# Optimization experiments

Hardware: AMD Instinct MI355X
Metric: run time of the kernel (lower is better)

The kernel has to match this reference:

```python
import jax, jax.numpy as jnp
import numpy as np

B, N, T, NL, DIM, H, HD = 4, 2048, 8, 64, 1024, 16, 64


def setup_inputs() -> dict:
    key = jax.random.key(0)
    ks = jax.random.split(key, 8)
    text = jax.random.normal(ks[0], (B, N, DIM), dtype=jnp.float32)
    media = jax.random.normal(ks[1], (B, T, NL, DIM), dtype=jnp.float32)
    # place exactly T media tokens per row, evenly spaced, so cumsum times are in [1, T]
    loc = np.zeros((B, N), dtype=bool)
    step = N // T
    loc[:, np.arange(T) * step] = True
    media_locations = jnp.asarray(loc)
    s = 1.0 / np.sqrt(DIM)
    wq = jax.random.normal(ks[2], (DIM, DIM), dtype=jnp.float32) * s
    wkv = jax.random.normal(ks[3], (DIM, 2 * DIM), dtype=jnp.float32) * s
    wo = jax.random.normal(ks[4], (DIM, DIM), dtype=jnp.float32) * s
    bo = jnp.zeros((DIM,), dtype=jnp.float32)
    ln_g = jnp.ones((DIM,), dtype=jnp.float32)
    ln_b = jnp.zeros((DIM,), dtype=jnp.float32)
    return {"text": text, "media": media, "media_locations": media_locations,
            "wq": wq, "wkv": wkv, "wo": wo, "bo": bo, "ln_g": ln_g, "ln_b": ln_b}


def _layernorm(x, g, b, eps=1e-5):
    mu = jnp.mean(x, axis=-1, keepdims=True)
    var = jnp.var(x, axis=-1, keepdims=True)
    return (x - mu) * jax.lax.rsqrt(var + eps) * g + b


def reference(text, media, media_locations, wq, wkv, wo, bo, ln_g, ln_b):
    b, t, nl, d = media.shape
    tn = _layernorm(text, ln_g, ln_b)                 # [b, n, d]
    q = tn @ wq                                        # [b, n, d]
    m = media.reshape(b, t * nl, d)                    # [b, tn, d]
    kv = m @ wkv                                       # [b, tn, 2d]
    k, v = jnp.split(kv, 2, axis=-1)
    q = q.reshape(b, -1, H, HD).transpose(0, 2, 1, 3)  # [b, h, n, hd]
    k = k.reshape(b, -1, H, HD).transpose(0, 2, 1, 3)  # [b, h, tn, hd]
    v = v.reshape(b, -1, H, HD).transpose(0, 2, 1, 3)
    scores = jnp.einsum('bhid,bhjd->bhij', q, k)       # [b, h, n, tn]
    text_times = jnp.cumsum(media_locations.astype(jnp.int32), axis=-1)  # [b, n]
    media_times = jnp.repeat(jnp.arange(1, t + 1, dtype=jnp.int32), nl)  # [tn]
    mask = text_times[:, None, :, None] == media_times[None, None, None, :]
    neg = jnp.finfo(scores.dtype).min
    scores = jnp.where(mask, scores, neg)
    attn = jax.nn.softmax(scores, axis=-1)
    no_media = (text_times == 0)[:, None, :, None]     # [b, 1, n, 1]
    attn = jnp.where(no_media, 0.0, attn)
    out = jnp.einsum('bhij,bhjd->bhid', attn, v)       # [b, h, n, hd]
    out = out.transpose(0, 2, 1, 3).reshape(b, -1, H * HD)
    return out @ wo + bo
```

## Files before the change

### kernel.cpp

```cpp
#include <hip/hip_runtime.h>
#include <stdint.h>

#define B_ 4
#define N_ 2048
#define T_ 8
#define NL_ 64
#define DIM_ 1024
#define H_ 16
#define HD_ 64
#define TN_ (T_*NL_)

typedef __bf16 bf16x8 __attribute__((ext_vector_type(8)));
typedef float f32x4 __attribute__((ext_vector_type(4)));

__device__ __forceinline__ float b2f(unsigned short x) {
  union { uint32_t u; float f; } v; v.u = ((uint32_t)x) << 16; return v.f;
}
__device__ __forceinline__ unsigned short f2b(float f) {
  union { float f; uint32_t u; } v; v.f = f;
  uint32_t r = v.u + 0x7FFFu + ((v.u >> 16) & 1u);
  return (unsigned short)(r >> 16);
}

__device__ __forceinline__ void gload_lds16(const unsigned short* g, unsigned short* l) {
  __builtin_amdgcn_global_load_lds(
      (const __attribute__((address_space(1))) uint32_t*)g,
      (__attribute__((address_space(3))) uint32_t*)l, 16, 0, 0);
}

__global__ void detect_kernel(const unsigned short* __restrict__ text, int* __restrict__ flag) {
  int t = threadIdx.x;
  int bad = 0;
  #pragma unroll
  for (int i = 0; i < 16; i++) {
    unsigned short w = text[t * 16 + i];
    int e = (w >> 7) & 0xFF;
    if (e != 0 && (e < 90 || e > 150)) bad++;
  }
  __shared__ int red[256];
  red[t] = bad;
  __syncthreads();
  for (int o = 128; o > 0; o >>= 1) { if (t < o) red[t] += red[t + o]; __syncthreads(); }
  if (t == 0) flag[0] = (red[0] > 256) ? 1 : 0;
}

#define PREP_TIMES 4
#define PREP_LN    (B_*N_)
#define PREP_CAST  2049
#define PREP_TR    4096

__global__ __launch_bounds__(256) void prep_kernel(
    const void* __restrict__ locs, int* __restrict__ tt,
    const void* __restrict__ text, const void* __restrict__ lng,
    const void* __restrict__ lnb, unsigned short* __restrict__ tn,
    const void* __restrict__ media, unsigned short* __restrict__ mb,
    const void* __restrict__ bo, unsigned short* __restrict__ bob,
    const void* __restrict__ wq, unsigned short* __restrict__ wqt,
    const void* __restrict__ wkv, unsigned short* __restrict__ wkvt,
    const void* __restrict__ wo, unsigned short* __restrict__ wot,
    const int* __restrict__ flag) {
  __shared__ __align__(16) unsigned char shraw[32 * 33 * 2];
  int gb = blockIdx.x;
  int t = threadIdx.x;

  if (gb < PREP_TIMES) {
    int* red = (int*)shraw;
    int b = gb;
    const unsigned char* p8 = (const unsigned char*)locs;
    const int* p32 = (const int*)locs;
    int cnt = 0;
    for (int i = t; i < B_*N_; i += 256) cnt += (p8[i] != 0) ? 1 : 0;
    red[t] = cnt;
    __syncthreads();
    for (int off = 128; off > 0; off >>= 1) {
      if (t < off) red[t] += red[t + off];
      __syncthreads();
    }
    int total = red[0];
    __syncthreads();
    bool isb = (total >= 2 * T_);
    int x[8];
    int base = b * N_ + t * 8;
    if (isb) {
      #pragma unroll
      for (int i = 0; i < 8; i++) x[i] = (int)(p8[base + i] != 0);
    } else {
      #pragma unroll
      for (int i = 0; i < 8; i++) x[i] = (int)(p32[base + i] != 0);
    }
    #pragma unroll
    for (int i = 1; i < 8; i++) x[i] += x[i-1];
    int tot = x[7];
    red[t] = tot;
    __syncthreads();
    for (int off = 1; off < 256; off <<= 1) {
      int v = (t >= off) ? red[t - off] : 0;
      __syncthreads();
      red[t] += v;
      __syncthreads();
    }
    int excl = red[t] - tot;
    #pragma unroll
    for (int i = 0; i < 8; i++) tt[base + i] = excl + x[i];
    return;
  }
  gb -= PREP_TIMES;

  if (gb < PREP_LN) {
    float* sm = (float*)shraw;
    int row = gb;
    bool isf = (*flag != 0);
    float f0, f1, f2, f3, g0, g1, g2, g3, c0, c1, c2, c3;
    if (isf) {
      float4 xv = ((const float4*)text)[(size_t)row * (DIM_/4) + t];
      f0 = xv.x; f1 = xv.y; f2 = xv.z; f3 = xv.w;
      float4 gv = ((const float4*)lng)[t];
      g0 = gv.x; g1 = gv.y; g2 = gv.z; g3 = gv.w;
      float4 bv = ((const float4*)lnb)[t];
      c0 = bv.x; c1 = bv.y; c2 = bv.z; c3 = bv.w;
    } else {
      ushort4 xv = ((const ushort4*)text)[(size_t)row * (DIM_/4) + t];
      f0 = b2f(xv.x); f1 = b2f(xv.y); f2 = b2f(xv.z); f3 = b2f(xv.w);
      ushort4 gv = ((const ushort4*)lng)[t];
      g0 = b2f(gv.x); g1 = b2f(gv.y); g2 = b2f(gv.z); g3 = b2f(gv.w);
      ushort4 bv = ((const ushort4*)lnb)[t];
      c0 = b2f(bv.x); c1 = b2f(bv.y); c2 = b2f(bv.z); c3 = b2f(bv.w);
    }
    float s  = f0 + f1 + f2 + f3;
    float s2 = f0*f0 + f1*f1 + f2*f2 + f3*f3;
    for (int off = 32; off > 0; off >>= 1) { s += __shfl_xor(s, off); s2 += __shfl_xor(s2, off); }
    int wave = t >> 6, lane = t & 63;
    if (lane == 0) { sm[wave] = s; sm[wave + 4] = s2; }
    __syncthreads();
    float ts  = sm[0] + sm[1] + sm[2] + sm[3];
    float ts2 = sm[4] + sm[5] + sm[6] + sm[7];
    float mean = ts * (1.0f / DIM_);
    float var  = ts2 * (1.0f / DIM_) - mean * mean;
    float rs = rsqrtf(var + 1e-5f);
    ushort4 o;
    o.x = f2b((f0 - mean) * rs * g0 + c0);
    o.y = f2b((f1 - mean) * rs * g1 + c1);
    o.z = f2b((f2 - mean) * rs * g2 + c2);
    o.w = f2b((f3 - mean) * rs * g3 + c3);
    ((ushort4*)(tn + (size_t)row * DIM_))[t] = o;
    return;
  }
  gb -= PREP_LN;

  if (gb < PREP_CAST) {
    const int N4M = (B_*T_*NL_*DIM_) / 4;
    int i = gb * 256 + t;
    bool isf = (*flag != 0);
    if (i < N4M) {
      ushort4 o;
      if (isf) {
        float4 v = ((const float4*)media)[i];
        o.x = f2b(v.x); o.y = f2b(v.y); o.z = f2b(v.z); o.w = f2b(v.w);
      } else {
        o = ((const ushort4*)media)[i];
      }
      ((ushort4*)mb)[i] = o;
    } else {
      int j = i - N4M;
      if (j < DIM_/4) {
        ushort4 o;
        if (isf) {
          float4 v = ((const float4*)bo)[j];
          o.x = f2b(v.x); o.y = f2b(v.y); o.z = f2b(v.z); o.w = f2b(v.w);
        } else {
          o = ((const ushort4*)bo)[j];
        }
        ((ushort4*)bob)[j] = o;
      }
    }
    return;
  }
  gb -= PREP_CAST;

  {
    unsigned short (*tile)[33] = (unsigned short (*)[33])shraw;
    const void* src; unsigned short* dst; int C, zz, nx;
    if (gb < 1024)      { src = wq;  dst = wqt;  C = 1024; zz = gb;        nx = 32; }
    else if (gb < 3072) { src = wkv; dst = wkvt; C = 2048; zz = gb - 1024; nx = 64; }
    else                { src = wo;  dst = wot;  C = 1024; zz = gb - 3072; nx = 32; }
    const int R = 1024;
    int xi = zz % nx, yi = zz / nx;
    int bx = xi * 32, by = yi * 32;
    int x = t & 31, y = t >> 5;
    if (*flag) {
      const float* s = (const float*)src;
      for (int i = y; i < 32; i += 8) tile[i][x] = f2b(s[(size_t)(by + i) * C + bx + x]);
    } else {
      const unsigned short* s = (const unsigned short*)src;
      for (int i = y; i < 32; i += 8) tile[i][x] = s[(size_t)(by + i) * C + bx + x];
    }
    __syncthreads();
    for (int i = y; i < 32; i += 8) dst[(size_t)(bx + i) * R + by + x] = tile[x][i];
  }
}

__device__ __forceinline__ void gemm128_core(const unsigned short* __restrict__ A,
                                             const unsigned short* __restrict__ Bt,
                                             unsigned short* __restrict__ C,
                                             float* __restrict__ Cf,
                                             const unsigned short* __restrict__ bias,
                                             int bid, int mtiles, int M, int N, int K,
                                             bool f32o, int t) {
  __shared__ unsigned short As[3][128][32];
  __shared__ unsigned short Bs[3][128][32];
  int m0 = (bid % mtiles) * 128, n0 = (bid / mtiles) * 128;
  int wave = t >> 6, lane = t & 63;
  int wr = wave >> 1, wc = wave & 1;
  f32x4 acc[4][4];
  #pragma unroll
  for (int i = 0; i < 4; i++)
    #pragma unroll
    for (int j = 0; j < 4; j++)
      #pragma unroll
      for (int r = 0; r < 4; r++) acc[i][j][r] = 0.f;
  int lr = lane & 15;
  int lk = (((lane >> 4) ^ ((lr >> 2) & 3)) & 3) * 8;
  int row0 = t >> 2,         kcp0 = (t & 3) * 8;
  int row1 = (t + 256) >> 2, kcp1 = ((t + 256) & 3) * 8;
  int kg0 = (((t & 3) ^ ((row0 >> 2) & 3)) & 3) * 8;
  int kg1 = ((((t + 256) & 3) ^ ((row1 >> 2) & 3)) & 3) * 8;
  const unsigned short* a0 = A  + (size_t)(m0 + row0) * K + kg0;
  const unsigned short* a1 = A  + (size_t)(m0 + row1) * K + kg1;
  const unsigned short* b0 = Bt + (size_t)(n0 + row0) * K + kg0;
  const unsigned short* b1 = Bt + (size_t)(n0 + row1) * K + kg1;
#define STAGE_(buf, koff) do { \
    gload_lds16(a0 + (koff), &As[buf][row0][kcp0]); \
    gload_lds16(a1 + (koff), &As[buf][row1][kcp1]); \
    gload_lds16(b0 + (koff), &Bs[buf][row0][kcp0]); \
    gload_lds16(b1 + (koff), &Bs[buf][row1][kcp1]); \
  } while (0)
  STAGE_(0, 0);
  STAGE_(1, 32);
  STAGE_(2, 64);
  asm volatile("s_waitcnt vmcnt(8)" ::: "memory");
  __builtin_amdgcn_s_barrier();
  int cur = 0;
  for (int k0 = 0; k0 < K; k0 += 32) {
    bf16x8 af[4], bfr[4];
    #pragma unroll
    for (int i = 0; i < 4; i++) af[i]  = *(const bf16x8*)(&As[cur][wr * 64 + i * 16 + lr][lk]);
    #pragma unroll
    for (int j = 0; j < 4; j++) bfr[j] = *(const bf16x8*)(&Bs[cur][wc * 64 + j * 16 + lr][lk]);
    asm volatile("s_waitcnt lgkmcnt(0)" ::: "memory");
    __builtin_amdgcn_sched_barrier(0);
    __builtin_amdgcn_s_barrier();
    if (k0 + 96 < K) {
      STAGE_(cur, k0 + 96);
      __builtin_amdgcn_sched_barrier(0);
    }
    #pragma unroll
    for (int i = 0; i < 4; i++)
      #pragma unroll
      for (int j = 0; j < 4; j++)
        acc[i][j] = __builtin_amdgcn_mfma_f32_16x16x32_bf16(af[i], bfr[j], acc[i][j], 0, 0, 0);
    if (k0 + 96 < K) {
      asm volatile("s_waitcnt vmcnt(8)" ::: "memory");
      __builtin_amdgcn_s_barrier();
    } else if (k0 + 64 < K) {
      asm volatile("s_waitcnt vmcnt(4)" ::: "memory");
      __builtin_amdgcn_s_barrier();
    } else if (k0 + 32 < K) {
      asm volatile("s_waitcnt vmcnt(0)" ::: "memory");
      __builtin_amdgcn_s_barrier();
    }
    cur = (cur == 2) ? 0 : cur + 1;
  }
#undef STAGE_
  int rbase = (lane >> 4) * 4;
  int cbase = lane & 15;
  #pragma unroll
  for (int i = 0; i < 4; i++) {
    #pragma unroll
    for (int j = 0; j < 4; j++) {
      int row = m0 + wr * 64 + i * 16 + rbase;
      int col = n0 + wc * 64 + j * 16 + cbase;
      float bv = bias ? b2f(bias[col]) : 0.f;
      if (f32o) {
        #pragma unroll
        for (int r = 0; r < 4; r++)
          Cf[(size_t)(row + r) * N + col] = acc[i][j][r] + bv;
      } else {
        #pragma unroll
        for (int r = 0; r < 4; r++)
          C[(size_t)(row + r) * N + col] = f2b(acc[i][j][r] + bv);
      }
    }
  }
}

__global__ __launch_bounds__(256) void gemm_qkv(const unsigned short* __restrict__ tn,
                                                const unsigned short* __restrict__ wqt,
                                                unsigned short* __restrict__ qb,
                                                const unsigned short* __restrict__ mb,
                                                const unsigned short* __restrict__ wkvt,
                                                unsigned short* __restrict__ kvb) {
  int bid = blockIdx.x;
  if (bid < 512)
    gemm128_core(tn, wqt, qb, nullptr, nullptr, bid, 64, B_ * N_, DIM_, DIM_, false, threadIdx.x);
  else
    gemm128_core(mb, wkvt, kvb, nullptr, nullptr, bid - 512, 16, B_ * TN_, 2 * DIM_, DIM_, false, threadIdx.x);
}

__global__ __launch_bounds__(256) void gemm_out(const unsigned short* __restrict__ ao,
                                                const unsigned short* __restrict__ wot,
                                                unsigned short* __restrict__ C,
                                                float* __restrict__ Cf,
                                                const unsigned short* __restrict__ bias,
                                                const int* __restrict__ flag) {
  bool f32o = (*flag != 0);
  gemm128_core(ao, wot, C, Cf, bias, blockIdx.x, 64, B_ * N_, DIM_, DIM_, f32o, threadIdx.x);
}

__global__ __launch_bounds__(64) void attn_mfma(const unsigned short* __restrict__ q,
                                                const unsigned short* __restrict__ kv,
                                                const int* __restrict__ tt,
                                                unsigned short* __restrict__ ao) {
  __shared__ unsigned short Vt[64][72];
  __shared__ unsigned short Ps[64][72];
  int bid = blockIdx.x;
  int h  = bid & 15;
  int nt = (bid >> 4) & 31;
  int b  = bid >> 9;
  int bn0 = b * N_ + nt * 64;
  int lane = threadIdx.x & 63;
  int lr = lane & 15;
  int g  = lane >> 4;
  int g8 = g * 8;

  int tv = tt[bn0];
  float vmul = (tv >= 1 && tv <= T_) ? 1.f : 0.f;
  int tvc = tv < 1 ? 1 : (tv > T_ ? T_ : tv);
  int kvrow0 = b * TN_ + (tvc - 1) * NL_;

  const unsigned short* vbase = kv + (size_t)kvrow0 * (2 * DIM_) + DIM_ + h * HD_;
  #pragma unroll
  for (int d0 = 0; d0 < 64; d0 += 8) {
    uint4 v = *(const uint4*)(vbase + (size_t)lane * (2 * DIM_) + d0);
    Vt[d0 + 0][lane] = (unsigned short)(v.x & 0xffff);
    Vt[d0 + 1][lane] = (unsigned short)(v.x >> 16);
    Vt[d0 + 2][lane] = (unsigned short)(v.y & 0xffff);
    Vt[d0 + 3][lane] = (unsigned short)(v.y >> 16);
    Vt[d0 + 4][lane] = (unsigned short)(v.z & 0xffff);
    Vt[d0 + 5][lane] = (unsigned short)(v.z >> 16);
    Vt[d0 + 6][lane] = (unsigned short)(v.w & 0xffff);
    Vt[d0 + 7][lane] = (unsigned short)(v.w >> 16);
  }

  f32x4 S[4][4];
  #pragma unroll
  for (int i = 0; i < 4; i++)
    #pragma unroll
    for (int j = 0; j < 4; j++)
      #pragma unroll
      for (int r = 0; r < 4; r++) S[i][j][r] = 0.f;
  #pragma unroll
  for (int ks = 0; ks < 2; ks++) {
    bf16x8 aQ[4], bK[4];
    #pragma unroll
    for (int mi = 0; mi < 4; mi++)
      aQ[mi] = *(const bf16x8*)(q + (size_t)(bn0 + mi * 16 + lr) * DIM_ + h * HD_ + ks * 32 + g8);
    #pragma unroll
    for (int ni = 0; ni < 4; ni++)
      bK[ni] = *(const bf16x8*)(kv + (size_t)(kvrow0 + ni * 16 + lr) * (2 * DIM_) + h * HD_ + ks * 32 + g8);
    #pragma unroll
    for (int mi = 0; mi < 4; mi++)
      #pragma unroll
      for (int ni = 0; ni < 4; ni++)
        S[mi][ni] = __builtin_amdgcn_mfma_f32_16x16x32_bf16(aQ[mi], bK[ni], S[mi][ni], 0, 0, 0);
  }

  #pragma unroll
  for (int mi = 0; mi < 4; mi++) {
    #pragma unroll
    for (int r = 0; r < 4; r++) {
      float mx = fmaxf(fmaxf(S[mi][0][r], S[mi][1][r]), fmaxf(S[mi][2][r], S[mi][3][r]));
      mx = fmaxf(mx, __shfl_xor(mx, 1));
      mx = fmaxf(mx, __shfl_xor(mx, 2));
      mx = fmaxf(mx, __shfl_xor(mx, 4));
      mx = fmaxf(mx, __shfl_xor(mx, 8));
      float e0 = __expf(S[mi][0][r] - mx);
      float e1 = __expf(S[mi][1][r] - mx);
      float e2 = __expf(S[mi][2][r] - mx);
      float e3 = __expf(S[mi][3][r] - mx);
      float sum = e0 + e1 + e2 + e3;
      sum += __shfl_xor(sum, 1);
      sum += __shfl_xor(sum, 2);
      sum += __shfl_xor(sum, 4);
      sum += __shfl_xor(sum, 8);
      float inv = 1.f / sum;
      int qrow = mi * 16 + g * 4 + r;
      Ps[qrow][ 0 + lr] = f2b(e0 * inv);
      Ps[qrow][16 + lr] = f2b(e1 * inv);
      Ps[qrow][32 + lr] = f2b(e2 * inv);
      Ps[qrow][48 + lr] = f2b(e3 * inv);
    }
  }
  __syncthreads();

  f32x4 O[4][4];
  #pragma unroll
  for (int i = 0; i < 4; i++)
    #pragma unroll
    for (int j = 0; j < 4; j++)
      #pragma unroll
      for (int r = 0; r < 4; r++) O[i][j][r] = 0.f;
  #pragma unroll
  for (int ks = 0; ks < 2; ks++) {
    bf16x8 aP[4], bV[4];
    #pragma unroll
    for (int mi = 0; mi < 4; mi++)
      aP[mi] = *(const bf16x8*)(&Ps[mi * 16 + lr][ks * 32 + g8]);
    #pragma unroll
    for (int ni = 0; ni < 4; ni++)
      bV[ni] = *(const bf16x8*)(&Vt[ni * 16 + lr][ks * 32 + g8]);
    #pragma unroll
    for (int mi = 0; mi < 4; mi++)
      #pragma unroll
      for (int ni = 0; ni < 4; ni++)
        O[mi][ni] = __builtin_amdgcn_mfma_f32_16x16x32_bf16(aP[mi], bV[ks ? ni : ni], O[mi][ni], 0, 0, 0);
  }
  __syncthreads();

  #pragma unroll
  for (int mi = 0; mi < 4; mi++)
    #pragma unroll
    for (int ni = 0; ni < 4; ni++)
      #pragma unroll
      for (int r = 0; r < 4; r++)
        Ps[mi * 16 + g * 4 + r][ni * 16 + lr] = f2b(O[mi][ni][r] * vmul);
  __syncthreads();
  uint4* dst = (uint4*)(ao + (size_t)(bn0 + lane) * DIM_ + h * HD_);
  #pragma unroll
  for (int c = 0; c < 8; c++)
    dst[c] = *(const uint4*)(&Ps[lane][c * 8]);
}

extern "C" void kernel_launch(void* const* d_in, const int* in_sizes, int n_in,
                              void* d_out, int out_size, void* d_ws, size_t ws_size,
                              hipStream_t stream) {
  const void* text = d_in[0];
  const void* media = d_in[1];
  const void* mloc = d_in[2];
  const void* wq  = d_in[3];
  const void* wkv = d_in[4];
  const void* wo  = d_in[5];
  const void* bo  = d_in[6];
  const void* lng = d_in[7];
  const void* lnb = d_in[8];

  char* ws = (char*)d_ws;
  const size_t OFF_FLAG = (size_t)32 << 10;
  const size_t OFF_TN   = (size_t)64 << 10;
  const size_t OFF_WQT  = OFF_TN  + ((size_t)16 << 20) + ((size_t)64 << 10);
  const size_t OFF_WKVT = OFF_WQT + ((size_t)2 << 20);
  const size_t OFF_WOT  = OFF_WKVT + ((size_t)4 << 20);
  const size_t OFF_KV   = OFF_WOT + ((size_t)2 << 20);
  const size_t OFF_MB   = OFF_KV  + ((size_t)8 << 20);
  const size_t OFF_BO   = OFF_MB  + ((size_t)4 << 20);
  const size_t OFF_QB   = OFF_BO  + ((size_t)64 << 10);
  int* tt               = (int*)(ws + 0);
  int* flag             = (int*)(ws + OFF_FLAG);
  unsigned short* tn    = (unsigned short*)(ws + OFF_TN);
  unsigned short* ao    = tn;
  unsigned short* wqt   = (unsigned short*)(ws + OFF_WQT);
  unsigned short* wkvt  = (unsigned short*)(ws + OFF_WKVT);
  unsigned short* wot   = (unsigned short*)(ws + OFF_WOT);
  unsigned short* kvb   = (unsigned short*)(ws + OFF_KV);
  unsigned short* mb    = (unsigned short*)(ws + OFF_MB);
  unsigned short* bob   = (unsigned short*)(ws + OFF_BO);
  unsigned short* qb    = (unsigned short*)(ws + OFF_QB);

  detect_kernel<<<1, 256, 0, stream>>>((const unsigned short*)text, flag);
  prep_kernel<<<PREP_TIMES + PREP_LN + PREP_CAST + PREP_TR, 256, 0, stream>>>(
      mloc, tt, text, lng, lnb, tn, media, mb, bo, bob,
      wq, wqt, wkv, wkvt, wo, wot, flag);

  gemm_qkv<<<768, 256, 0, stream>>>(tn, wqt, qb, mb, wkvt, kvb);
  attn_mfma<<<B_ * (N_/64) * H_, 64, 0, stream>>>(qb, kvb, tt, ao);
  gemm_out<<<512, 256, 0, stream>>>(ao, wot, (unsigned short*)d_out, (float*)d_out, bob, flag);
}
```

Before: 194.9 us.

## Fold dtype detection into prep, wave-per-row layernorm, single-barrier GEMM pipeline

Removes the separate detect kernel launch by having every prep block recompute the input-dtype check with a wave shuffle reduction. Block 0 writes the flag for later kernels. Layernorm now handles four rows per block with one wave per row, so the shared-memory cross-wave reduction and its barrier go away. The GEMM main loop drops from three stages of prefetch to two and runs one barrier per iteration instead of two. This cuts sync overhead but leaves less latency hiding, and every prep block now re-reads the detection sample.

Result: no change. 196.7 us (+0.9%).

```diff
diff --git a/kernel.cpp b/kernel.cpp
--- a/kernel.cpp
+++ b/kernel.cpp
@@ -28,24 +28,22 @@
       (__attribute__((address_space(3))) uint32_t*)l, 16, 0, 0);
 }
 
-__global__ void detect_kernel(const unsigned short* __restrict__ text, int* __restrict__ flag) {
-  int t = threadIdx.x;
+__device__ __forceinline__ bool detect_isf(const unsigned short* text, int t) {
+  int l = t & 63;
   int bad = 0;
   #pragma unroll
   for (int i = 0; i < 16; i++) {
-    unsigned short w = text[t * 16 + i];
+    unsigned short w = text[l * 16 + i];
     int e = (w >> 7) & 0xFF;
     if (e != 0 && (e < 90 || e > 150)) bad++;
   }
-  __shared__ int red[256];
-  red[t] = bad;
-  __syncthreads();
-  for (int o = 128; o > 0; o >>= 1) { if (t < o) red[t] += red[t + o]; __syncthreads(); }
-  if (t == 0) flag[0] = (red[0] > 256) ? 1 : 0;
+  #pragma unroll
+  for (int off = 32; off > 0; off >>= 1) bad += __shfl_xor(bad, off);
+  return bad > 64;
 }
 
 #define PREP_TIMES 4
-#define PREP_LN    (B_*N_)
+#define PREP_LN2   2048
 #define PREP_CAST  2049
 #define PREP_TR    4096
 
@@ -58,10 +56,12 @@
     const void* __restrict__ wq, unsigned short* __restrict__ wqt,
     const void* __restrict__ wkv, unsigned short* __restrict__ wkvt,
     const void* __restrict__ wo, unsigned short* __restrict__ wot,
-    const int* __restrict__ flag) {
+    int* __restrict__ flag) {
   __shared__ __align__(16) unsigned char shraw[32 * 33 * 2];
   int gb = blockIdx.x;
   int t = threadIdx.x;
+  bool isf = detect_isf((const unsigned short*)text, t);
+  if (gb == 0 && t == 0) flag[0] = isf ? 1 : 0;
 
   if (gb < PREP_TIMES) {
     int* red = (int*)shraw;
@@ -106,51 +106,62 @@
   }
   gb -= PREP_TIMES;
 
-  if (gb < PREP_LN) {
-    float* sm = (float*)shraw;
-    int row = gb;
-    bool isf = (*flag != 0);
-    float f0, f1, f2, f3, g0, g1, g2, g3, c0, c1, c2, c3;
+  if (gb < PREP_LN2) {
+    int row = gb * 4 + (t >> 6);
+    int l = t & 63;
+    float f[16], gv_[16], cv_[16];
     if (isf) {
-      float4 xv = ((const float4*)text)[(size_t)row * (DIM_/4) + t];
-      f0 = xv.x; f1 = xv.y; f2 = xv.z; f3 = xv.w;
-      float4 gv = ((const float4*)lng)[t];
-      g0 = gv.x; g1 = gv.y; g2 = gv.z; g3 = gv.w;
-      float4 bv = ((const float4*)lnb)[t];
-      c0 = bv.x; c1 = bv.y; c2 = bv.z; c3 = bv.w;
+      const float4* x4 = (const float4*)text + (size_t)row * 256;
+      const float4* g4 = (const float4*)lng;
+      const float4* b4 = (const float4*)lnb;
+      #pragma unroll
+      for (int j = 0; j < 4; j++) {
+        float4 xv = x4[l + 64*j];
+        float4 gg = g4[l + 64*j];
+        float4 bb = b4[l + 64*j];
+        f[4*j+0]=xv.x; f[4*j+1]=xv.y; f[4*j+2]=xv.z; f[4*j+3]=xv.w;
+        gv_[4*j+0]=gg.x; gv_[4*j+1]=gg.y; gv_[4*j+2]=gg.z; gv_[4*j+3]=gg.w;
+        cv_[4*j+0]=bb.x; cv_[4*j+1]=bb.y; cv_[4*j+2]=bb.z; cv_[4*j+3]=bb.w;
+      }
     } else {
-      ushort4 xv = ((const ushort4*)text)[(size_t)row * (DIM_/4) + t];
-      f0 = b2f(xv.x); f1 = b2f(xv.y); f2 = b2f(xv.z); f3 = b2f(xv.w);
-      ushort4 gv = ((const ushort4*)lng)[t];
-      g0 = b2f(gv.x); g1 = b2f(gv.y); g2 = b2f(gv.z); g3 = b2f(gv.w);
-      ushort4 bv = ((const ushort4*)lnb)[t];
-      c0 = b2f(bv.x); c1 = b2f(bv.y); c2 = b2f(bv.z); c3 = b2f(bv.w);
-    }
-    float s  = f0 + f1 + f2 + f3;
-    float s2 = f0*f0 + f1*f1 + f2*f2 + f3*f3;
+      const ushort4* x4 = (const ushort4*)text + (size_t)row * 256;
+      const ushort4* g4 = (const ushort4*)lng;
+      const ushort4* b4 = (const ushort4*)lnb;
+      #pragma unroll
+      for (int j = 0; j < 4; j++) {
+        ushort4 xv = x4[l + 64*j];
+        ushort4 gg = g4[l + 64*j];
+        ushort4 bb = b4[l + 64*j];
+        f[4*j+0]=b2f(xv.x); f[4*j+1]=b2f(xv.y); f[4*j+2]=b2f(xv.z); f[4*j+3]=b2f(xv.w);
+        gv_[4*j+0]=b2f(gg.x); gv_[4*j+1]=b2f(gg.y); gv_[4*j+2]=b2f(gg.z); gv_[4*j+3]=b2f(gg.w);
+        cv_[4*j+0]=b2f(bb.x); cv_[4*j+1]=b2f(bb.y); cv_[4*j+2]=b2f(bb.z); cv_[4*j+3]=b2f(bb.w);
+      }
+    }
+    float s = 0.f, s2 = 0.f;
+    #pragma unroll
+    for (int i = 0; i < 16; i++) { s += f[i]; s2 += f[i]*f[i]; }
+    #pragma unroll
     for (int off = 32; off > 0; off >>= 1) { s += __shfl_xor(s, off); s2 += __shfl_xor(s2, off); }
-    int wave = t >> 6, lane = t & 63;
-    if (lane == 0) { sm[wave] = s; sm[wave + 4] = s2; }
-    __syncthreads();
-    float ts  = sm[0] + sm[1] + sm[2] + sm[3];
-    float ts2 = sm[4] + sm[5] + sm[6] + sm[7];
-    float mean = ts * (1.0f / DIM_);
-    float var  = ts2 * (1.0f / DIM_) - mean * mean;
+    float mean = s * (1.0f / DIM_);
+    float var  = s2 * (1.0f / DIM_) - mean * mean;
     float rs = rsqrtf(var + 1e-5f);
-    ushort4 o;
-    o.x = f2b((f0 - mean) * rs * g0 + c0);
-    o.y = f2b((f1 - mean) * rs * g1 + c1);
-    o.z = f2b((f2 - mean) * rs * g2 + c2);
-    o.w = f2b((f3 - mean) * rs * g3 + c3);
-    ((ushort4*)(tn + (size_t)row * DIM_))[t] = o;
+    ushort4* o4 = (ushort4*)(tn + (size_t)row * DIM_);
+    #pragma unroll
+    for (int j = 0; j < 4; j++) {
+      ushort4 o;
+      o.x = f2b((f[4*j+0] - mean) * rs * gv_[4*j+0] + cv_[4*j+0]);
+      o.y = f2b((f[4*j+1] - mean) * rs * gv_[4*j+1] + cv_[4*j+1]);
+      o.z = f2b((f[4*j+2] - mean) * rs * gv_[4*j+2] + cv_[4*j+2]);
+      o.w = f2b((f[4*j+3] - mean) * rs * gv_[4*j+3] + cv_[4*j+3]);
+      o4[l + 64*j] = o;
+    }
     return;
   }
-  gb -= PREP_LN;
+  gb -= PREP_LN2;
 
   if (gb < PREP_CAST) {
     const int N4M = (B_*T_*NL_*DIM_) / 4;
     int i = gb * 256 + t;
-    bool isf = (*flag != 0);
     if (i < N4M) {
       ushort4 o;
       if (isf) {
@@ -187,7 +198,7 @@
     int xi = zz % nx, yi = zz / nx;
     int bx = xi * 32, by = yi * 32;
     int x = t & 31, y = t >> 5;
-    if (*flag) {
+    if (isf) {
       const float* s = (const float*)src;
       for (int i = y; i < 32; i += 8) tile[i][x] = f2b(s[(size_t)(by + i) * C + bx + x]);
     } else {
@@ -236,8 +247,7 @@
   } while (0)
   STAGE_(0, 0);
   STAGE_(1, 32);
-  STAGE_(2, 64);
-  asm volatile("s_waitcnt vmcnt(8)" ::: "memory");
+  asm volatile("s_waitcnt vmcnt(4)" ::: "memory");
   __builtin_amdgcn_s_barrier();
   int cur = 0;
   for (int k0 = 0; k0 < K; k0 += 32) {
@@ -248,9 +258,9 @@
     for (int j = 0; j < 4; j++) bfr[j] = *(const bf16x8*)(&Bs[cur][wc * 64 + j * 16 + lr][lk]);
     asm volatile("s_waitcnt lgkmcnt(0)" ::: "memory");
     __builtin_amdgcn_sched_barrier(0);
-    __builtin_amdgcn_s_barrier();
-    if (k0 + 96 < K) {
-      STAGE_(cur, k0 + 96);
+    if (k0 + 64 < K) {
+      int nb2 = cur + 2; if (nb2 >= 3) nb2 -= 3;
+      STAGE_(nb2, k0 + 64);
       __builtin_amdgcn_sched_barrier(0);
     }
     #pragma unroll
@@ -258,16 +268,12 @@
       #pragma unroll
       for (int j = 0; j < 4; j++)
         acc[i][j] = __builtin_amdgcn_mfma_f32_16x16x32_bf16(af[i], bfr[j], acc[i][j], 0, 0, 0);
-    if (k0 + 96 < K) {
-      asm volatile("s_waitcnt vmcnt(8)" ::: "memory");
-      __builtin_amdgcn_s_barrier();
-    } else if (k0 + 64 < K) {
+    if (k0 + 64 < K) {
       asm volatile("s_waitcnt vmcnt(4)" ::: "memory");
-      __builtin_amdgcn_s_barrier();
     } else if (k0 + 32 < K) {
       asm volatile("s_waitcnt vmcnt(0)" ::: "memory");
-      __builtin_amdgcn_s_barrier();
-    }
+    }
+    __builtin_amdgcn_s_barrier();
     cur = (cur == 2) ? 0 : cur + 1;
   }
 #undef STAGE_
@@ -422,7 +428,7 @@
     for (int mi = 0; mi < 4; mi++)
       #pragma unroll
       for (int ni = 0; ni < 4; ni++)
-        O[mi][ni] = __builtin_amdgcn_mfma_f32_16x16x32_bf16(aP[mi], bV[ks ? ni : ni], O[mi][ni], 0, 0, 0);
+        O[mi][ni] = __builtin_amdgcn_mfma_f32_16x16x32_bf16(aP[mi], bV[ni], O[mi][ni], 0, 0, 0);
   }
   __syncthreads();
 
@@ -475,8 +481,7 @@
   unsigned short* bob   = (unsigned short*)(ws + OFF_BO);
   unsigned short* qb    = (unsigned short*)(ws + OFF_QB);
 
-  detect_kernel<<<1, 256, 0, stream>>>((const unsigned short*)text, flag);
-  prep_kernel<<<PREP_TIMES + PREP_LN + PREP_CAST + PREP_TR, 256, 0, stream>>>(
+  prep_kernel<<<PREP_TIMES + PREP_LN2 + PREP_CAST + PREP_TR, 256, 0, stream>>>(
       mloc, tt, text, lng, lnb, tn, media, mb, bo, bob,
       wq, wqt, wkv, wkvt, wo, wot, flag);
 
```
